# Kernel tuning notes

Measured on AMD Instinct MI355X. Metric: run time of the kernel, lower is better.

The kernel has to match this reference:

```python
import jax, jax.numpy as jnp
import numpy as np

N = 50000      # nodes
E = 800000     # edges
F_NODE = 64
PE = 16
F_EDGE = 16
H = 128        # hidden_dim
L = 4          # num_layers
G = 64         # graphs in batch
NC = 10        # num_classes
BN_EPS = 1e-5


def _bn(h, g, b):
    # BatchNorm1d with batch statistics (deterministic train-style stats, no dropout)
    m = jnp.mean(h, axis=0)
    v = jnp.var(h, axis=0)
    return (h - m) * jax.lax.rsqrt(v + BN_EPS) * g + b


def setup_inputs() -> dict:
    key = jax.random.key(0)
    ks = jax.random.split(key, 16)
    p = lambda k, shape: (jax.random.normal(k, shape, jnp.float32) * 0.05)
    return dict(
        x=jax.random.normal(ks[0], (N, F_NODE), jnp.float32),
        pe=jax.random.normal(ks[1], (N, PE), jnp.float32),
        edge_index=jax.random.randint(ks[2], (2, E), 0, N),
        edge_attr=jax.random.normal(ks[3], (E, F_EDGE), jnp.float32),
        batch=jnp.sort(jax.random.randint(ks[4], (N,), 0, G)),
        W_in=p(ks[5], (F_NODE + PE, H)), b_in=jnp.zeros((H,), jnp.float32),
        We_edge=p(ks[6], (L, F_EDGE, H)), be_edge=jnp.zeros((L, H), jnp.float32),
        eps=jnp.zeros((L,), jnp.float32),
        W1_gin=p(ks[7], (L, H, 2 * H)), b1_gin=jnp.zeros((L, 2 * H), jnp.float32),
        W2_gin=p(ks[8], (L, 2 * H, H)), b2_gin=jnp.zeros((L, H), jnp.float32),
        bn1_g=jnp.ones((L, H), jnp.float32), bn1_b=jnp.zeros((L, H), jnp.float32),
        W1_ffn=p(ks[9], (L, H, 2 * H)), b1_ffn=jnp.zeros((L, 2 * H), jnp.float32),
        W2_ffn=p(ks[10], (L, 2 * H, H)), b2_ffn=jnp.zeros((L, H), jnp.float32),
        bn2_g=jnp.ones((L, H), jnp.float32), bn2_b=jnp.zeros((L, H), jnp.float32),
        W_r1=p(ks[11], (H, H)), b_r1=jnp.zeros((H,), jnp.float32),
        W_r2=p(ks[12], (H, NC)), b_r2=jnp.zeros((NC,), jnp.float32),
    )


def reference(x, pe, edge_index, edge_attr, batch,
              W_in, b_in, We_edge, be_edge, eps,
              W1_gin, b1_gin, W2_gin, b2_gin, bn1_g, bn1_b,
              W1_ffn, b1_ffn, W2_ffn, b2_ffn, bn2_g, bn2_b,
              W_r1, b_r1, W_r2, b_r2):
    src, dst = edge_index[0], edge_index[1]  # PyG: row=source j, col=target i
    # input projection on [x || pe]
    h = jax.nn.relu(jnp.concatenate([x, pe], axis=-1) @ W_in + b_in)  # [N,H]
    for l in range(L):
        # --- GINEConv: msg = relu(x_j + lin_edge(e_ij)); sum-aggregate to target
        e = edge_attr @ We_edge[l] + be_edge[l]                        # [E,H]
        msg = jax.nn.relu(h[src] + e)                                  # gather + fuse
        agg = jax.ops.segment_sum(msg, dst, num_segments=N)           # scatter-add
        z = (1.0 + eps[l]) * h + agg
        z = jax.nn.relu(z @ W1_gin[l] + b1_gin[l]) @ W2_gin[l] + b2_gin[l]
        # --- GNNPlusLayer: BN -> ReLU -> residual (identity proj, in==out)
        z = jax.nn.relu(_bn(z, bn1_g[l], bn1_b[l]))
        z = z + h
        # --- FFN (eval mode): out = lin2(relu(lin1(z))) + z, then BN
        f = jax.nn.relu(z @ W1_ffn[l] + b1_ffn[l]) @ W2_ffn[l] + b2_ffn[l]
        h = _bn(f + z, bn2_g[l], bn2_b[l])
    # --- global mean pool over graphs
    sums = jax.ops.segment_sum(h, batch, num_segments=G)               # [G,H]
    counts = jax.ops.segment_sum(jnp.ones((N,), h.dtype), batch, num_segments=G)
    hg = sums / jnp.maximum(counts, 1.0)[:, None]
    # --- readout MLP (dropout off in eval)
    return jax.nn.relu(hg @ W_r1 + b_r1) @ W_r2 + b_r2                 # [G,NC]
```

## Files before the change

### kernel.cpp

```cpp
#include <hip/hip_runtime.h>
#include <hip/hip_bf16.h>

#define NN 50000
#define NE 800000
#define FIN 80
#define H 128
#define H2 256
#define NG 64
#define NCLS 10
#define BN_EPS 1e-5f
#define NB 196
#define LDK 40
#define LDY 264

typedef __attribute__((ext_vector_type(8))) short bf16x8;
typedef __attribute__((ext_vector_type(8))) unsigned short us8;
typedef __attribute__((ext_vector_type(4))) float f32x4;

__device__ __forceinline__ unsigned short f2b(float f) {
    __hip_bfloat16 h = __float2bfloat16(f);
    return *(unsigned short*)&h;
}
__device__ __forceinline__ float b2f(unsigned short u) {
    unsigned v = (unsigned)u << 16;
    return __uint_as_float(v);
}

__global__ void wprep_all(const float* __restrict__ W1g, const float* __restrict__ W2g,
                          const float* __restrict__ W1f, const float* __restrict__ W2f,
                          unsigned short* __restrict__ wt)
{
    const int idx = blockIdx.x * 256 + threadIdx.x;
    const int m = idx >> 17;
    const int r = idx & 131071;
    const float* W;
    unsigned short* Wt;
    int K, Nn;
    if (m == 0)      { W = W1g; Wt = wt;              K = 128; Nn = 256; }
    else if (m == 1) { W = W2g; Wt = wt + 4 * 65536;  K = 256; Nn = 128; }
    else if (m == 2) { W = W1f; Wt = wt + 8 * 65536;  K = 128; Nn = 256; }
    else             { W = W2f; Wt = wt + 12 * 65536; K = 256; Nn = 128; }
    const int per = K * Nn;
    const int l = r / per;
    const int rr = r - l * per;
    const int k = rr / Nn;
    const int n = rr - k * Nn;
    const float wv = W[r];
    const unsigned short hi = f2b(wv);
    const unsigned short lo = f2b(wv - b2f(hi));
    const int KB = K >> 5;
    const int kb = k >> 5, kk = k & 31;
    unsigned short* base = Wt + (size_t)l * 2 * per;
    base[((size_t)(0 * KB + kb) * Nn + n) * 32 + kk] = hi;
    base[((size_t)(1 * KB + kb) * Nn + n) * 32 + kk] = lo;
}

template<bool ZF>
__global__ __launch_bounds__(256, 2)
void gemm_pair(const float* __restrict__ Ain, const float* __restrict__ hres,
               const unsigned short* __restrict__ Wt1, const unsigned short* __restrict__ Wt2,
               const float* __restrict__ b1, const float* __restrict__ b2,
               const float* __restrict__ statsIn, const float* __restrict__ bng,
               const float* __restrict__ bnb, float* __restrict__ statsOut,
               float* __restrict__ Cout, float inv_n, int M)
{
    __shared__ unsigned short sA[128][LDK];
    __shared__ unsigned short sy[128][LDY];
    __shared__ float sAB[128];
    __shared__ float sSH[128];

    const int tid = threadIdx.x;
    const int m0 = blockIdx.x * 128;
    const int lane = tid & 63;
    const int w = tid >> 6;
    const int fr = lane & 15;
    const int fq = (lane >> 4) * 8;
    const int crow4 = (lane >> 4) * 4;
    const int arow = tid >> 1;
    const int akh = (tid & 1) * 16;
    const int gm = m0 + arow;

    if (ZF) {
        if (tid < 128) {
            float su = 0.f, qu = 0.f;
#pragma unroll
            for (int s = 0; s < 8; ++s) {
                su += statsIn[s * 256 + tid];
                qu += statsIn[s * 256 + 128 + tid];
            }
            const float mean = su * inv_n;
            const float var = qu * inv_n - mean * mean;
            const float a = bng[tid] * rsqrtf(var + BN_EPS);
            sAB[tid] = a;
            sSH[tid] = fmaf(-mean, a, bnb[tid]);
        }
    }

    f32x4 acc1[2][16];
#pragma unroll
    for (int r = 0; r < 2; ++r)
#pragma unroll
        for (int c = 0; c < 16; ++c) acc1[r][c] = (f32x4)(0.f);

    for (int kb = 0; kb < 4; ++kb) {
        __syncthreads();
        if (gm < M) {
            const float* tf = Ain + (size_t)gm * 128 + kb * 32 + akh;
            float zv[16];
            if (ZF) {
                const float* hf = hres + (size_t)gm * 128 + kb * 32 + akh;
#pragma unroll
                for (int i = 0; i < 16; ++i) {
                    const int c = kb * 32 + akh + i;
                    zv[i] = fmaxf(fmaf(tf[i], sAB[c], sSH[c]), 0.f) + hf[i];
                }
            } else {
#pragma unroll
                for (int i = 0; i < 16; ++i) zv[i] = tf[i];
            }
            us8 p0, p1;
#pragma unroll
            for (int i = 0; i < 8; ++i) { p0[i] = f2b(zv[i]); p1[i] = f2b(zv[8 + i]); }
            *(us8*)&sA[arow][akh]     = p0;
            *(us8*)&sA[arow][akh + 8] = p1;
        } else {
            *(float4*)&sA[arow][akh]     = make_float4(0.f, 0.f, 0.f, 0.f);
            *(float4*)&sA[arow][akh + 8] = make_float4(0.f, 0.f, 0.f, 0.f);
        }
        __syncthreads();
        const bf16x8 a0 = *(const bf16x8*)&sA[w * 32 + fr][fq];
        const bf16x8 a1 = *(const bf16x8*)&sA[w * 32 + 16 + fr][fq];
#pragma unroll
        for (int ct = 0; ct < 16; ++ct) {
            const bf16x8 bh = *(const bf16x8*)&Wt1[((size_t)(kb) * 256 + ct * 16 + fr) * 32 + fq];
            const bf16x8 bl = *(const bf16x8*)&Wt1[((size_t)(4 + kb) * 256 + ct * 16 + fr) * 32 + fq];
            acc1[0][ct] = __builtin_amdgcn_mfma_f32_16x16x32_bf16(a0, bh, acc1[0][ct], 0, 0, 0);
            acc1[0][ct] = __builtin_amdgcn_mfma_f32_16x16x32_bf16(a0, bl, acc1[0][ct], 0, 0, 0);
            acc1[1][ct] = __builtin_amdgcn_mfma_f32_16x16x32_bf16(a1, bh, acc1[1][ct], 0, 0, 0);
            acc1[1][ct] = __builtin_amdgcn_mfma_f32_16x16x32_bf16(a1, bl, acc1[1][ct], 0, 0, 0);
        }
    }
#pragma unroll
    for (int ct = 0; ct < 16; ++ct) {
        const float bb = b1[ct * 16 + fr];
#pragma unroll
        for (int r = 0; r < 2; ++r) {
            const int row0 = w * 32 + r * 16 + crow4;
#pragma unroll
            for (int reg = 0; reg < 4; ++reg) {
                const float o = fmaxf(acc1[r][ct][reg] + bb, 0.f);
                sy[row0 + reg][ct * 16 + fr] = f2b(o);
            }
        }
    }
    __syncthreads();

    f32x4 acc2[2][8];
#pragma unroll
    for (int r = 0; r < 2; ++r)
#pragma unroll
        for (int c = 0; c < 8; ++c) acc2[r][c] = (f32x4)(0.f);

    for (int kb = 0; kb < 8; ++kb) {
        const bf16x8 ya0 = *(const bf16x8*)&sy[w * 32 + fr][kb * 32 + fq];
        const bf16x8 ya1 = *(const bf16x8*)&sy[w * 32 + 16 + fr][kb * 32 + fq];
#pragma unroll
        for (int ct = 0; ct < 8; ++ct) {
            const bf16x8 bh = *(const bf16x8*)&Wt2[((size_t)(kb) * 128 + ct * 16 + fr) * 32 + fq];
            const bf16x8 bl = *(const bf16x8*)&Wt2[((size_t)(8 + kb) * 128 + ct * 16 + fr) * 32 + fq];
            acc2[0][ct] = __builtin_amdgcn_mfma_f32_16x16x32_bf16(ya0, bh, acc2[0][ct], 0, 0, 0);
            acc2[0][ct] = __builtin_amdgcn_mfma_f32_16x16x32_bf16(ya0, bl, acc2[0][ct], 0, 0, 0);
            acc2[1][ct] = __builtin_amdgcn_mfma_f32_16x16x32_bf16(ya1, bh, acc2[1][ct], 0, 0, 0);
            acc2[1][ct] = __builtin_amdgcn_mfma_f32_16x16x32_bf16(ya1, bl, acc2[1][ct], 0, 0, 0);
        }
    }

    float s[8], q[8];
#pragma unroll
    for (int c = 0; c < 8; ++c) { s[c] = 0.f; q[c] = 0.f; }
#pragma unroll
    for (int r = 0; r < 2; ++r) {
        const int rbase = m0 + w * 32 + r * 16 + crow4;
#pragma unroll
        for (int ct = 0; ct < 8; ++ct) {
            const int gc = ct * 16 + fr;
            const float bb = b2[gc];
#pragma unroll
            for (int reg = 0; reg < 4; ++reg) {
                const int gr = rbase + reg;
                if (gr >= M) continue;
                float o = acc2[r][ct][reg] + bb;
                if (ZF) {
                    const float tv = Ain[(size_t)gr * 128 + gc];
                    const float hv = hres[(size_t)gr * 128 + gc];
                    o += fmaxf(fmaf(tv, sAB[gc], sSH[gc]), 0.f) + hv;
                }
                s[ct] += o;
                q[ct] = fmaf(o, o, q[ct]);
                Cout[(size_t)gr * 128 + gc] = o;
            }
        }
    }

#pragma unroll
    for (int c = 0; c < 8; ++c) {
        s[c] += __shfl_xor(s[c], 32, 64); s[c] += __shfl_xor(s[c], 16, 64);
        q[c] += __shfl_xor(q[c], 32, 64); q[c] += __shfl_xor(q[c], 16, 64);
    }
    __syncthreads();
    float* red = (float*)sA;
    if (lane < 16) {
#pragma unroll
        for (int c = 0; c < 8; ++c) {
            red[w * 128 + c * 16 + lane]       = s[c];
            red[512 + w * 128 + c * 16 + lane] = q[c];
        }
    }
    __syncthreads();
    if (tid < 128) {
        const float ss = red[tid] + red[128 + tid] + red[256 + tid] + red[384 + tid];
        const float qq = red[512 + tid] + red[640 + tid] + red[768 + tid] + red[896 + tid];
        float* slab = statsOut + (blockIdx.x & 7) * 256;
        atomicAdd(&slab[tid], ss);
        atomicAdd(&slab[128 + tid], qq);
    }
}

__global__ __launch_bounds__(256, 4)
void inproj_kernel(const float* __restrict__ x, const float* __restrict__ pe,
                   const float* __restrict__ W, const float* __restrict__ bias,
                   float* __restrict__ C, unsigned short* __restrict__ Cb, int M)
{
    __shared__ float aT[16][129];
    __shared__ float wsh[16][129];

    const int tid = threadIdx.x;
    const int m0 = blockIdx.x * 128;
    const int rm = (tid >> 4) * 8;
    const int rn = (tid & 15) * 8;

    float acc[8][8];
#pragma unroll
    for (int i = 0; i < 8; ++i)
#pragma unroll
        for (int j = 0; j < 8; ++j) acc[i][j] = 0.f;

    const int lm = tid & 127;
    const int kq = (tid >> 7) * 8;
    const int wk = tid >> 4;
    const int wj = (tid & 15) * 8;

    for (int k0 = 0; k0 < FIN; k0 += 16) {
        {
            const int gm = m0 + lm;
            const int c = k0 + kq;
            if (gm < M) {
                const float* srcp = (c < 64) ? (x + (size_t)gm * 64 + c)
                                             : (pe + (size_t)gm * 16 + (c - 64));
                const float4 v0 = *(const float4*)srcp;
                const float4 v1 = *(const float4*)(srcp + 4);
                aT[kq + 0][lm] = v0.x; aT[kq + 1][lm] = v0.y;
                aT[kq + 2][lm] = v0.z; aT[kq + 3][lm] = v0.w;
                aT[kq + 4][lm] = v1.x; aT[kq + 5][lm] = v1.y;
                aT[kq + 6][lm] = v1.z; aT[kq + 7][lm] = v1.w;
            } else {
#pragma unroll
                for (int i = 0; i < 8; ++i) aT[kq + i][lm] = 0.f;
            }
        }
        {
#pragma unroll
            for (int j = 0; j < 8; ++j)
                wsh[wk][wj + j] = W[(size_t)(k0 + wk) * H + wj + j];
        }
        __syncthreads();
#pragma unroll
        for (int k = 0; k < 16; ++k) {
            const float av[8] = {aT[k][rm], aT[k][rm + 1], aT[k][rm + 2], aT[k][rm + 3],
                                 aT[k][rm + 4], aT[k][rm + 5], aT[k][rm + 6], aT[k][rm + 7]};
            const float bv[8] = {wsh[k][rn], wsh[k][rn + 1], wsh[k][rn + 2], wsh[k][rn + 3],
                                 wsh[k][rn + 4], wsh[k][rn + 5], wsh[k][rn + 6], wsh[k][rn + 7]};
#pragma unroll
            for (int i = 0; i < 8; ++i)
#pragma unroll
                for (int j = 0; j < 8; ++j)
                    acc[i][j] = fmaf(av[i], bv[j], acc[i][j]);
        }
        __syncthreads();
    }

    float bv[8];
#pragma unroll
    for (int j = 0; j < 8; ++j) bv[j] = bias[rn + j];
#pragma unroll
    for (int i = 0; i < 8; ++i) {
        const int gm = m0 + rm + i;
        if (gm >= M) continue;
        float o[8];
#pragma unroll
        for (int j = 0; j < 8; ++j) o[j] = fmaxf(acc[i][j] + bv[j], 0.f);
        *(float4*)&C[(size_t)gm * H + rn]     = make_float4(o[0], o[1], o[2], o[3]);
        *(float4*)&C[(size_t)gm * H + rn + 4] = make_float4(o[4], o[5], o[6], o[7]);
        us8 pk;
#pragma unroll
        for (int j = 0; j < 8; ++j) pk[j] = f2b(o[j]);
        *(us8*)&Cb[(size_t)gm * H + rn] = pk;
    }
}

__global__ void hist_kernel(const int* __restrict__ ei, int* __restrict__ deg)
{
    const int e = blockIdx.x * 256 + threadIdx.x;
    if (e < NE) atomicAdd(&deg[ei[NE + e]], 1);
}

__global__ void bsum_kernel(const int* __restrict__ deg, int* __restrict__ bsum)
{
    const int tid = threadIdx.x;
    const int i = blockIdx.x * 256 + tid;
    int v = (i < NN) ? deg[i] : 0;
#pragma unroll
    for (int off = 32; off > 0; off >>= 1) v += __shfl_down(v, off, 64);
    __shared__ int ws[4];
    if ((tid & 63) == 0) ws[tid >> 6] = v;
    __syncthreads();
    if (tid == 0) bsum[blockIdx.x] = ws[0] + ws[1] + ws[2] + ws[3];
}

__global__ void bscan_kernel(int* __restrict__ bsum)
{
    __shared__ int sh[256];
    const int tid = threadIdx.x;
    sh[tid] = (tid < NB) ? bsum[tid] : 0;
    __syncthreads();
    for (int off = 1; off < 256; off <<= 1) {
        const int t = (tid >= off) ? sh[tid - off] : 0;
        __syncthreads();
        sh[tid] += t;
        __syncthreads();
    }
    if (tid < NB) bsum[tid] = (tid == 0) ? 0 : sh[tid - 1];
}

__global__ void bwrite_kernel(const int* __restrict__ deg, const int* __restrict__ boff,
                              int* __restrict__ rowptr, int* __restrict__ cursor)
{
    __shared__ int sh[256];
    const int tid = threadIdx.x;
    const int i = blockIdx.x * 256 + tid;
    const int v = (i < NN) ? deg[i] : 0;
    sh[tid] = v;
    __syncthreads();
    for (int off = 1; off < 256; off <<= 1) {
        const int t = (tid >= off) ? sh[tid - off] : 0;
        __syncthreads();
        sh[tid] += t;
        __syncthreads();
    }
    if (i < NN) {
        const int pos = boff[blockIdx.x] + sh[tid] - v;
        rowptr[i] = pos;
        cursor[i] = pos;
    }
    if (blockIdx.x == 0 && tid == 0) rowptr[NN] = NE;
}

__global__ void scat_idx(const int* __restrict__ ei, int* __restrict__ cursor,
                         int* __restrict__ src_s, int* __restrict__ perm)
{
    const int e = blockIdx.x * 256 + threadIdx.x;
    if (e >= NE) return;
    const int pos = atomicAdd(&cursor[ei[NE + e]], 1);
    src_s[pos] = ei[e];
    perm[pos] = e;
}

__global__ void gather_ea(const float* __restrict__ ea, const int* __restrict__ perm,
                          float* __restrict__ ea_s)
{
    const int idx = blockIdx.x * 256 + threadIdx.x;
    const int pos = idx >> 2;
    const int qd = idx & 3;
    const int e = perm[pos];
    *(float4*)&ea_s[(size_t)pos * 16 + qd * 4] = *(const float4*)&ea[(size_t)e * 16 + qd * 4];
}

__global__ __launch_bounds__(256)
void agg_kernel(const float* __restrict__ h, const unsigned short* __restrict__ hb,
                const int* __restrict__ rowptr, const int* __restrict__ src_s,
                const float* __restrict__ ea_s, const float* __restrict__ We,
                const float* __restrict__ be, const float* __restrict__ eps, int l,
                float* __restrict__ z)
{
    const int lane = threadIdx.x & 63;
    const int w = threadIdx.x >> 6;
    const int n = blockIdx.x * 4 + w;
    if (n >= NN) return;

    float w0[16], w1[16];
#pragma unroll
    for (int k = 0; k < 16; ++k) {
        const float2 wv = *(const float2*)&We[k * H + 2 * lane];
        w0[k] = wv.x; w1[k] = wv.y;
    }
    const float2 bev = *(const float2*)&be[2 * lane];

    const int beg = __builtin_amdgcn_readfirstlane(rowptr[n]);
    const int end = __builtin_amdgcn_readfirstlane(rowptr[n + 1]);

    const float e1 = 1.0f + eps[l];
    const float2 hv0 = *(const float2*)&h[(size_t)n * H + 2 * lane];
    float acc0 = e1 * hv0.x;
    float acc1 = e1 * hv0.y;

    for (int i0 = beg; i0 < end; i0 += 16) {
        const int jn = min(16, end - i0);
        int srcs[16];
#pragma unroll
        for (int j = 0; j < 16; ++j)
            srcs[j] = src_s[(i0 + j < end) ? (i0 + j) : (end - 1)];
        unsigned hraw[16];
#pragma unroll
        for (int j = 0; j < 16; ++j)
            hraw[j] = *(const unsigned*)&hb[(size_t)srcs[j] * H + 2 * lane];
#pragma unroll
        for (int j = 0; j < 16; ++j) {
            if (j >= jn) break;
            const float* ar = ea_s + (size_t)(i0 + j) * 16;
            float s0 = bev.x, s1 = bev.y;
#pragma unroll
            for (int k = 0; k < 16; ++k) {
                const float a = ar[k];
                s0 = fmaf(a, w0[k], s0);
                s1 = fmaf(a, w1[k], s1);
            }
            const float hx = __uint_as_float(hraw[j] << 16);
            const float hy = __uint_as_float(hraw[j] & 0xffff0000u);
            acc0 += fmaxf(hx + s0, 0.f);
            acc1 += fmaxf(hy + s1, 0.f);
        }
    }
    *(float2*)&z[(size_t)n * H + 2 * lane] = make_float2(acc0, acc1);
}

__global__ void bn_apply_kernel(const float* __restrict__ u, const float* __restrict__ st,
                                const float* __restrict__ g, const float* __restrict__ b,
                                float* __restrict__ h, unsigned short* __restrict__ hb,
                                float inv_n)
{
    const int i = blockIdx.x * 256 + threadIdx.x;
    const int c = i & (H - 1);
    float su = 0.f, qu = 0.f;
#pragma unroll
    for (int s = 0; s < 8; ++s) { su += st[s * 256 + c]; qu += st[s * 256 + 128 + c]; }
    const float mean = su * inv_n;
    const float var = qu * inv_n - mean * mean;
    const float a = g[c] * rsqrtf(var + BN_EPS);
    const float sh = fmaf(-mean, a, b[c]);
    const float v = fmaf(u[i], a, sh);
    h[i] = v;
    hb[i] = f2b(v);
}

__global__ void pool_kernel(const float* __restrict__ h, const int* __restrict__ batch,
                            float* __restrict__ pool, float* __restrict__ cnt, int n)
{
    const int c = threadIdx.x & (H - 1);
    const int half = threadIdx.x >> 7;
    const int r0 = blockIdx.x * 256 + half * 128;
    if (r0 >= n) return;
    const int rend = min(r0 + 128, n);
    int gprev = batch[r0];
    float acc = 0.f;
    int run = 0;
    for (int r = r0; r < rend; ++r) {
        const int g = batch[r];
        if (g != gprev) {
            atomicAdd(&pool[gprev * H + c], acc);
            if (c == 0) atomicAdd(&cnt[gprev], (float)run);
            acc = 0.f; run = 0; gprev = g;
        }
        acc += h[(size_t)r * H + c];
        run++;
    }
    atomicAdd(&pool[gprev * H + c], acc);
    if (c == 0) atomicAdd(&cnt[gprev], (float)run);
}

__global__ void readout_kernel(const float* __restrict__ pool, const float* __restrict__ cnt,
                               const float* __restrict__ Wr1, const float* __restrict__ br1,
                               const float* __restrict__ Wr2, const float* __restrict__ br2,
                               float* __restrict__ out)
{
    __shared__ float hg[H];
    __shared__ float r1[H];
    const int g = blockIdx.x;
    const int j = threadIdx.x;
    hg[j] = pool[g * H + j] / fmaxf(cnt[g], 1.0f);
    __syncthreads();
    float acc = br1[j];
    for (int k = 0; k < H; ++k) acc = fmaf(hg[k], Wr1[k * H + j], acc);
    r1[j] = fmaxf(acc, 0.f);
    __syncthreads();
    if (j < NCLS) {
        float o = br2[j];
        for (int k = 0; k < H; ++k) o = fmaf(r1[k], Wr2[k * NCLS + j], o);
        out[g * NCLS + j] = o;
    }
}

extern "C" void kernel_launch(void* const* d_in, const int* in_sizes, int n_in,
                              void* d_out, int out_size, void* d_ws, size_t ws_size,
                              hipStream_t stream)
{
    const float* x       = (const float*)d_in[0];
    const float* pe      = (const float*)d_in[1];
    const int*   ei      = (const int*)d_in[2];
    const float* ea      = (const float*)d_in[3];
    const int*   batch   = (const int*)d_in[4];
    const float* W_in    = (const float*)d_in[5];
    const float* b_in    = (const float*)d_in[6];
    const float* We_edge = (const float*)d_in[7];
    const float* be_edge = (const float*)d_in[8];
    const float* eps     = (const float*)d_in[9];
    const float* W1g     = (const float*)d_in[10];
    const float* b1g     = (const float*)d_in[11];
    const float* W2g     = (const float*)d_in[12];
    const float* b2g     = (const float*)d_in[13];
    const float* bn1g    = (const float*)d_in[14];
    const float* bn1b    = (const float*)d_in[15];
    const float* W1f     = (const float*)d_in[16];
    const float* b1f     = (const float*)d_in[17];
    const float* W2f     = (const float*)d_in[18];
    const float* b2f     = (const float*)d_in[19];
    const float* bn2g    = (const float*)d_in[20];
    const float* bn2b    = (const float*)d_in[21];
    const float* Wr1     = (const float*)d_in[22];
    const float* br1     = (const float*)d_in[23];
    const float* Wr2     = (const float*)d_in[24];
    const float* br2     = (const float*)d_in[25];
    float* out = (float*)d_out;

    const size_t NH = (size_t)NN * H;
    float* hbuf  = (float*)d_ws;
    float* zbuf  = hbuf + NH;
    float* tbuf  = zbuf + NH;
    int*   perm  = (int*)(tbuf + NH);
    int*   deg   = perm + NE;
    float* stats = (float*)(deg + NN);
    float* pool  = stats + 16384;
    float* cnt   = pool + NG * H;
    int*   rowptr = (int*)(cnt + NG);
    int*   cursor = rowptr + NN + 1;
    int*   bsum   = cursor + NN;
    int*   src_s  = bsum + 256;
    float* ea_s   = (float*)(src_s + NE);
    unsigned short* hb = (unsigned short*)(ea_s + (size_t)NE * 16);
    unsigned short* wt = hb + NH;
    unsigned short* wt1g = wt;
    unsigned short* wt2g = wt + 4 * 65536;
    unsigned short* wt1f = wt + 8 * 65536;
    unsigned short* wt2f = wt + 12 * 65536;

    const dim3 blk(256);
    const dim3 mg1((NN + 127) / 128, 1);
    const int ew_grid = (int)(NH / 256);
    const float inv_n = 1.0f / (float)NN;
    const size_t zero_bytes = (size_t)(NN + 16384 + NG * H + NG) * 4;

    wprep_all<<<2048, blk, 0, stream>>>(W1g, W2g, W1f, W2f, wt);

    hipMemsetAsync(deg, 0, zero_bytes, stream);
    hist_kernel<<<(NE + 255) / 256, blk, 0, stream>>>(ei, deg);
    bsum_kernel<<<NB, blk, 0, stream>>>(deg, bsum);
    bscan_kernel<<<1, blk, 0, stream>>>(bsum);
    bwrite_kernel<<<NB, blk, 0, stream>>>(deg, bsum, rowptr, cursor);
    scat_idx<<<(NE + 255) / 256, blk, 0, stream>>>(ei, cursor, src_s, perm);
    gather_ea<<<(NE * 4) / 256, blk, 0, stream>>>(ea, perm, ea_s);

    inproj_kernel<<<mg1, blk, 0, stream>>>(x, pe, W_in, b_in, hbuf, hb, NN);

    for (int l = 0; l < 4; ++l) {
        float* s1 = stats + (size_t)l * 4096;
        float* s2 = s1 + 2048;

        agg_kernel<<<(NN + 3) / 4, blk, 0, stream>>>(hbuf, hb, rowptr, src_s, ea_s,
                                                     We_edge + (size_t)l * 16 * H,
                                                     be_edge + (size_t)l * H, eps, l, zbuf);

        gemm_pair<false><<<mg1, blk, 0, stream>>>(
            zbuf, nullptr, wt1g + (size_t)l * 65536, wt2g + (size_t)l * 65536,
            b1g + (size_t)l * H2, b2g + (size_t)l * H,
            nullptr, nullptr, nullptr, s1, tbuf, inv_n, NN);

        gemm_pair<true><<<mg1, blk, 0, stream>>>(
            tbuf, hbuf, wt1f + (size_t)l * 65536, wt2f + (size_t)l * 65536,
            b1f + (size_t)l * H2, b2f + (size_t)l * H,
            s1, bn1g + (size_t)l * H, bn1b + (size_t)l * H, s2, tbuf, inv_n, NN);

        bn_apply_kernel<<<ew_grid, blk, 0, stream>>>(tbuf, s2, bn2g + (size_t)l * H,
                                                     bn2b + (size_t)l * H, hbuf, hb, inv_n);
    }

    pool_kernel<<<(NN + 255) / 256, blk, 0, stream>>>(hbuf, batch, pool, cnt, NN);
    readout_kernel<<<NG, H, 0, stream>>>(pool, cnt, Wr1, br1, Wr2, br2, out);
}
```

Before: 1.146 ms.

## Shrink GEMM tile to 64 rows, store aggregation output as bf16

```diff
diff --git a/kernel.cpp b/kernel.cpp
--- a/kernel.cpp
+++ b/kernel.cpp
@@ -16,6 +16,7 @@
 typedef __attribute__((ext_vector_type(8))) short bf16x8;
 typedef __attribute__((ext_vector_type(8))) unsigned short us8;
 typedef __attribute__((ext_vector_type(4))) float f32x4;
+typedef __attribute__((ext_vector_type(2))) float f32x2;
 
 __device__ __forceinline__ unsigned short f2b(float f) {
     __hip_bfloat16 h = __float2bfloat16(f);
@@ -56,149 +57,136 @@
 }
 
 template<bool ZF>
-__global__ __launch_bounds__(256, 2)
-void gemm_pair(const float* __restrict__ Ain, const float* __restrict__ hres,
+__global__ __launch_bounds__(256, 3)
+void gemm_pair(const void* __restrict__ Ap, const float* __restrict__ hres,
                const unsigned short* __restrict__ Wt1, const unsigned short* __restrict__ Wt2,
                const float* __restrict__ b1, const float* __restrict__ b2,
                const float* __restrict__ statsIn, const float* __restrict__ bng,
                const float* __restrict__ bnb, float* __restrict__ statsOut,
                float* __restrict__ Cout, float inv_n, int M)
 {
-    __shared__ unsigned short sA[128][LDK];
-    __shared__ unsigned short sy[128][LDY];
+    __shared__ unsigned short sA[ZF ? 64 : 1][LDK];
+    __shared__ unsigned short sy[64][LDY];
     __shared__ float sAB[128];
     __shared__ float sSH[128];
 
     const int tid = threadIdx.x;
-    const int m0 = blockIdx.x * 128;
+    const int m0 = blockIdx.x * 64;
     const int lane = tid & 63;
     const int w = tid >> 6;
     const int fr = lane & 15;
     const int fq = (lane >> 4) * 8;
     const int crow4 = (lane >> 4) * 4;
-    const int arow = tid >> 1;
-    const int akh = (tid & 1) * 16;
-    const int gm = m0 + arow;
 
     if (ZF) {
-        if (tid < 128) {
+#pragma unroll
+        for (int rep = 0; rep < 2; ++rep) {
+            const int c = lane + rep * 64;
             float su = 0.f, qu = 0.f;
 #pragma unroll
             for (int s = 0; s < 8; ++s) {
-                su += statsIn[s * 256 + tid];
-                qu += statsIn[s * 256 + 128 + tid];
+                su += statsIn[s * 256 + c];
+                qu += statsIn[s * 256 + 128 + c];
             }
             const float mean = su * inv_n;
             const float var = qu * inv_n - mean * mean;
-            const float a = bng[tid] * rsqrtf(var + BN_EPS);
-            sAB[tid] = a;
-            sSH[tid] = fmaf(-mean, a, bnb[tid]);
-        }
-    }
-
-    f32x4 acc1[2][16];
-#pragma unroll
-    for (int r = 0; r < 2; ++r)
-#pragma unroll
-        for (int c = 0; c < 16; ++c) acc1[r][c] = (f32x4)(0.f);
+            const float a = bng[c] * rsqrtf(var + BN_EPS);
+            sAB[c] = a;
+            sSH[c] = fmaf(-mean, a, bnb[c]);
+        }
+    }
+
+    f32x4 acc1[16];
+#pragma unroll
+    for (int c = 0; c < 16; ++c) acc1[c] = (f32x4)(0.f);
+
+    const int arow = tid >> 2;
+    const int akq = (tid & 3) * 8;
 
     for (int kb = 0; kb < 4; ++kb) {
-        __syncthreads();
-        if (gm < M) {
-            const float* tf = Ain + (size_t)gm * 128 + kb * 32 + akh;
-            float zv[16];
-            if (ZF) {
-                const float* hf = hres + (size_t)gm * 128 + kb * 32 + akh;
-#pragma unroll
-                for (int i = 0; i < 16; ++i) {
-                    const int c = kb * 32 + akh + i;
-                    zv[i] = fmaxf(fmaf(tf[i], sAB[c], sSH[c]), 0.f) + hf[i];
+        bf16x8 a0;
+        if (ZF) {
+            const int gm = m0 + arow;
+            if (gm < M) {
+                const float* tf = (const float*)Ap + (size_t)gm * 128 + kb * 32 + akq;
+                const float* hf = hres + (size_t)gm * 128 + kb * 32 + akq;
+                const float4 t0 = *(const float4*)tf;
+                const float4 t1 = *(const float4*)(tf + 4);
+                const float4 h0 = *(const float4*)hf;
+                const float4 h1 = *(const float4*)(hf + 4);
+                const float tv[8] = {t0.x, t0.y, t0.z, t0.w, t1.x, t1.y, t1.z, t1.w};
+                const float hv[8] = {h0.x, h0.y, h0.z, h0.w, h1.x, h1.y, h1.z, h1.w};
+                us8 p;
+#pragma unroll
+                for (int i = 0; i < 8; ++i) {
+                    const int c = kb * 32 + akq + i;
+                    p[i] = f2b(fmaxf(fmaf(tv[i], sAB[c], sSH[c]), 0.f) + hv[i]);
                 }
+                *(us8*)&sA[arow][akq] = p;
             } else {
-#pragma unroll
-                for (int i = 0; i < 16; ++i) zv[i] = tf[i];
+                *(float4*)&sA[arow][akq] = make_float4(0.f, 0.f, 0.f, 0.f);
             }
-            us8 p0, p1;
-#pragma unroll
-            for (int i = 0; i < 8; ++i) { p0[i] = f2b(zv[i]); p1[i] = f2b(zv[8 + i]); }
-            *(us8*)&sA[arow][akh]     = p0;
-            *(us8*)&sA[arow][akh + 8] = p1;
+            a0 = *(const bf16x8*)&sA[w * 16 + fr][fq];
         } else {
-            *(float4*)&sA[arow][akh]     = make_float4(0.f, 0.f, 0.f, 0.f);
-            *(float4*)&sA[arow][akh + 8] = make_float4(0.f, 0.f, 0.f, 0.f);
-        }
-        __syncthreads();
-        const bf16x8 a0 = *(const bf16x8*)&sA[w * 32 + fr][fq];
-        const bf16x8 a1 = *(const bf16x8*)&sA[w * 32 + 16 + fr][fq];
-#pragma unroll
-        for (int ct = 0; ct < 16; ++ct) {
-            const bf16x8 bh = *(const bf16x8*)&Wt1[((size_t)(kb) * 256 + ct * 16 + fr) * 32 + fq];
-            const bf16x8 bl = *(const bf16x8*)&Wt1[((size_t)(4 + kb) * 256 + ct * 16 + fr) * 32 + fq];
-            acc1[0][ct] = __builtin_amdgcn_mfma_f32_16x16x32_bf16(a0, bh, acc1[0][ct], 0, 0, 0);
-            acc1[0][ct] = __builtin_amdgcn_mfma_f32_16x16x32_bf16(a0, bl, acc1[0][ct], 0, 0, 0);
-            acc1[1][ct] = __builtin_amdgcn_mfma_f32_16x16x32_bf16(a1, bh, acc1[1][ct], 0, 0, 0);
-            acc1[1][ct] = __builtin_amdgcn_mfma_f32_16x16x32_bf16(a1, bl, acc1[1][ct], 0, 0, 0);
-        }
-    }
-#pragma unroll
-    for (int ct = 0; ct < 16; ++ct) {
-        const float bb = b1[ct * 16 + fr];
-#pragma unroll
-        for (int r = 0; r < 2; ++r) {
-            const int row0 = w * 32 + r * 16 + crow4;
-#pragma unroll
-            for (int reg = 0; reg < 4; ++reg) {
-                const float o = fmaxf(acc1[r][ct][reg] + bb, 0.f);
-                sy[row0 + reg][ct * 16 + fr] = f2b(o);
-            }
-        }
-    }
-    __syncthreads();
-
-    f32x4 acc2[2][8];
-#pragma unroll
-    for (int r = 0; r < 2; ++r)
-#pragma unroll
-        for (int c = 0; c < 8; ++c) acc2[r][c] = (f32x4)(0.f);
+            const unsigned short* zp = (const unsigned short*)Ap +
+                                       (size_t)(m0 + w * 16 + fr) * 128 + kb * 32 + fq;
+            a0 = *(const bf16x8*)zp;
+        }
+#pragma unroll
+        for (int nt = 0; nt < 16; ++nt) {
+            const bf16x8 bh = *(const bf16x8*)&Wt1[((size_t)(kb) * 256 + nt * 16 + fr) * 32 + fq];
+            const bf16x8 bl = *(const bf16x8*)&Wt1[((size_t)(4 + kb) * 256 + nt * 16 + fr) * 32 + fq];
+            acc1[nt] = __builtin_amdgcn_mfma_f32_16x16x32_bf16(a0, bh, acc1[nt], 0, 0, 0);
+            acc1[nt] = __builtin_amdgcn_mfma_f32_16x16x32_bf16(a0, bl, acc1[nt], 0, 0, 0);
+        }
+    }
+
+#pragma unroll
+    for (int nt = 0; nt < 16; ++nt) {
+        const float bb = b1[nt * 16 + fr];
+#pragma unroll
+        for (int reg = 0; reg < 4; ++reg) {
+            const float o = fmaxf(acc1[nt][reg] + bb, 0.f);
+            sy[w * 16 + crow4 + reg][nt * 16 + fr] = f2b(o);
+        }
+    }
+
+    f32x4 acc2[8];
+#pragma unroll
+    for (int c = 0; c < 8; ++c) acc2[c] = (f32x4)(0.f);
 
     for (int kb = 0; kb < 8; ++kb) {
-        const bf16x8 ya0 = *(const bf16x8*)&sy[w * 32 + fr][kb * 32 + fq];
-        const bf16x8 ya1 = *(const bf16x8*)&sy[w * 32 + 16 + fr][kb * 32 + fq];
+        const bf16x8 ya = *(const bf16x8*)&sy[w * 16 + fr][kb * 32 + fq];
 #pragma unroll
         for (int ct = 0; ct < 8; ++ct) {
             const bf16x8 bh = *(const bf16x8*)&Wt2[((size_t)(kb) * 128 + ct * 16 + fr) * 32 + fq];
             const bf16x8 bl = *(const bf16x8*)&Wt2[((size_t)(8 + kb) * 128 + ct * 16 + fr) * 32 + fq];
-            acc2[0][ct] = __builtin_amdgcn_mfma_f32_16x16x32_bf16(ya0, bh, acc2[0][ct], 0, 0, 0);
-            acc2[0][ct] = __builtin_amdgcn_mfma_f32_16x16x32_bf16(ya0, bl, acc2[0][ct], 0, 0, 0);
-            acc2[1][ct] = __builtin_amdgcn_mfma_f32_16x16x32_bf16(ya1, bh, acc2[1][ct], 0, 0, 0);
-            acc2[1][ct] = __builtin_amdgcn_mfma_f32_16x16x32_bf16(ya1, bl, acc2[1][ct], 0, 0, 0);
+            acc2[ct] = __builtin_amdgcn_mfma_f32_16x16x32_bf16(ya, bh, acc2[ct], 0, 0, 0);
+            acc2[ct] = __builtin_amdgcn_mfma_f32_16x16x32_bf16(ya, bl, acc2[ct], 0, 0, 0);
         }
     }
 
     float s[8], q[8];
 #pragma unroll
     for (int c = 0; c < 8; ++c) { s[c] = 0.f; q[c] = 0.f; }
-#pragma unroll
-    for (int r = 0; r < 2; ++r) {
-        const int rbase = m0 + w * 32 + r * 16 + crow4;
-#pragma unroll
-        for (int ct = 0; ct < 8; ++ct) {
-            const int gc = ct * 16 + fr;
-            const float bb = b2[gc];
-#pragma unroll
-            for (int reg = 0; reg < 4; ++reg) {
-                const int gr = rbase + reg;
-                if (gr >= M) continue;
-                float o = acc2[r][ct][reg] + bb;
-                if (ZF) {
-                    const float tv = Ain[(size_t)gr * 128 + gc];
-                    const float hv = hres[(size_t)gr * 128 + gc];
-                    o += fmaxf(fmaf(tv, sAB[gc], sSH[gc]), 0.f) + hv;
-                }
-                s[ct] += o;
-                q[ct] = fmaf(o, o, q[ct]);
-                Cout[(size_t)gr * 128 + gc] = o;
+    const int rbase = m0 + w * 16 + crow4;
+#pragma unroll
+    for (int ct = 0; ct < 8; ++ct) {
+        const int gc = ct * 16 + fr;
+        const float bb = b2[gc];
+#pragma unroll
+        for (int reg = 0; reg < 4; ++reg) {
+            const int gr = rbase + reg;
+            if (gr >= M) continue;
+            float o = acc2[ct][reg] + bb;
+            if (ZF) {
+                const float tv = ((const float*)Ap)[(size_t)gr * 128 + gc];
+                const float hv = hres[(size_t)gr * 128 + gc];
+                o += fmaxf(fmaf(tv, sAB[gc], sSH[gc]), 0.f) + hv;
             }
+            s[ct] += o;
+            q[ct] = fmaf(o, o, q[ct]);
+            Cout[(size_t)gr * 128 + gc] = o;
         }
     }
 
@@ -208,7 +196,7 @@
         q[c] += __shfl_xor(q[c], 32, 64); q[c] += __shfl_xor(q[c], 16, 64);
     }
     __syncthreads();
-    float* red = (float*)sA;
+    float* red = (float*)sy;
     if (lane < 16) {
 #pragma unroll
         for (int c = 0; c < 8; ++c) {
@@ -390,28 +378,24 @@
                 const int* __restrict__ rowptr, const int* __restrict__ src_s,
                 const float* __restrict__ ea_s, const float* __restrict__ We,
                 const float* __restrict__ be, const float* __restrict__ eps, int l,
-                float* __restrict__ z)
+                unsigned short* __restrict__ zb)
 {
     const int lane = threadIdx.x & 63;
     const int w = threadIdx.x >> 6;
     const int n = blockIdx.x * 4 + w;
     if (n >= NN) return;
 
-    float w0[16], w1[16];
-#pragma unroll
-    for (int k = 0; k < 16; ++k) {
-        const float2 wv = *(const float2*)&We[k * H + 2 * lane];
-        w0[k] = wv.x; w1[k] = wv.y;
-    }
-    const float2 bev = *(const float2*)&be[2 * lane];
+    f32x2 wv[16];
+#pragma unroll
+    for (int k = 0; k < 16; ++k)
+        wv[k] = *(const f32x2*)&We[k * H + 2 * lane];
+    const f32x2 bev = *(const f32x2*)&be[2 * lane];
 
     const int beg = __builtin_amdgcn_readfirstlane(rowptr[n]);
     const int end = __builtin_amdgcn_readfirstlane(rowptr[n + 1]);
 
     const float e1 = 1.0f + eps[l];
-    const float2 hv0 = *(const float2*)&h[(size_t)n * H + 2 * lane];
-    float acc0 = e1 * hv0.x;
-    float acc1 = e1 * hv0.y;
+    f32x2 acc = (*(const f32x2*)&h[(size_t)n * H + 2 * lane]) * e1;
 
     for (int i0 = beg; i0 < end; i0 += 16) {
         const int jn = min(16, end - i0);
@@ -427,20 +411,19 @@
         for (int j = 0; j < 16; ++j) {
             if (j >= jn) break;
             const float* ar = ea_s + (size_t)(i0 + j) * 16;
-            float s0 = bev.x, s1 = bev.y;
-#pragma unroll
-            for (int k = 0; k < 16; ++k) {
-                const float a = ar[k];
-                s0 = fmaf(a, w0[k], s0);
-                s1 = fmaf(a, w1[k], s1);
-            }
-            const float hx = __uint_as_float(hraw[j] << 16);
-            const float hy = __uint_as_float(hraw[j] & 0xffff0000u);
-            acc0 += fmaxf(hx + s0, 0.f);
-            acc1 += fmaxf(hy + s1, 0.f);
-        }
-    }
-    *(float2*)&z[(size_t)n * H + 2 * lane] = make_float2(acc0, acc1);
+            f32x2 s2 = bev;
+#pragma unroll
+            for (int k = 0; k < 16; ++k)
+                s2 = __builtin_elementwise_fma((f32x2)(ar[k]), wv[k], s2);
+            f32x2 hv = {__uint_as_float(hraw[j] << 16),
+                        __uint_as_float(hraw[j] & 0xffff0000u)};
+            f32x2 m = hv + s2;
+            m = __builtin_elementwise_max(m, (f32x2)(0.f));
+            acc += m;
+        }
+    }
+    const unsigned u = ((unsigned)f2b(acc[1]) << 16) | (unsigned)f2b(acc[0]);
+    *(unsigned*)&zb[(size_t)n * H + 2 * lane] = u;
 }
 
 __global__ void bn_apply_kernel(const float* __restrict__ u, const float* __restrict__ st,
@@ -543,9 +526,9 @@
 
     const size_t NH = (size_t)NN * H;
     float* hbuf  = (float*)d_ws;
-    float* zbuf  = hbuf + NH;
-    float* tbuf  = zbuf + NH;
-    int*   perm  = (int*)(tbuf + NH);
+    float* tbuf  = hbuf + NH;
+    unsigned short* zb = (unsigned short*)(tbuf + NH);
+    int*   perm  = (int*)(zb + NH);
     int*   deg   = perm + NE;
     float* stats = (float*)(deg + NN);
     float* pool  = stats + 16384;
@@ -563,7 +546,8 @@
     unsigned short* wt2f = wt + 12 * 65536;
 
     const dim3 blk(256);
-    const dim3 mg1((NN + 127) / 128, 1);
+    const dim3 ip_g((NN + 127) / 128, 1);
+    const dim3 gp_g((NN + 63) / 64, 1);
     const int ew_grid = (int)(NH / 256);
     const float inv_n = 1.0f / (float)NN;
     const size_t zero_bytes = (size_t)(NN + 16384 + NG * H + NG) * 4;
@@ -578,7 +562,7 @@
     scat_idx<<<(NE + 255) / 256, blk, 0, stream>>>(ei, cursor, src_s, perm);
     gather_ea<<<(NE * 4) / 256, blk, 0, stream>>>(ea, perm, ea_s);
 
-    inproj_kernel<<<mg1, blk, 0, stream>>>(x, pe, W_in, b_in, hbuf, hb, NN);
+    inproj_kernel<<<ip_g, blk, 0, stream>>>(x, pe, W_in, b_in, hbuf, hb, NN);
 
     for (int l = 0; l < 4; ++l) {
         float* s1 = stats + (size_t)l * 4096;
@@ -586,14 +570,14 @@
 
         agg_kernel<<<(NN + 3) / 4, blk, 0, stream>>>(hbuf, hb, rowptr, src_s, ea_s,
                                                      We_edge + (size_t)l * 16 * H,
-                                                     be_edge + (size_t)l * H, eps, l, zbuf);
-
-        gemm_pair<false><<<mg1, blk, 0, stream>>>(
-            zbuf, nullptr, wt1g + (size_t)l * 65536, wt2g + (size_t)l * 65536,
+                                                     be_edge + (size_t)l * H, eps, l, zb);
+
+        gemm_pair<false><<<gp_g, blk, 0, stream>>>(
+            zb, nullptr, wt1g + (size_t)l * 65536, wt2g + (size_t)l * 65536,
             b1g + (size_t)l * H2, b2g + (size_t)l * H,
             nullptr, nullptr, nullptr, s1, tbuf, inv_n, NN);
 
-        gemm_pair<true><<<mg1, blk, 0, stream>>>(
+        gemm_pair<true><<<gp_g, blk, 0, stream>>>(
             tbuf, hbuf, wt1f + (size_t)l * 65536, wt2f + (size_t)l * 65536,
             b1f + (size_t)l * H2, b2f + (size_t)l * H,
             s1, bn1g + (size_t)l * H, bn1b + (size_t)l * H, s2, tbuf, inv_n, NN);
```

After: 1.388 ms. 21.1% more time.
